# Performance work log

Measured on AMD Instinct MI355X. Metric: run time of the kernel, lower is better.

Reference implementation:

```python
import jax, jax.numpy as jnp
import numpy as np

N, M, D = 256, 64, 1024


def _l2norm(x, axis=-1, eps=1e-12):
    # tf.math.l2_normalize semantics: x / sqrt(max(sum(x^2), eps))
    sq = jnp.sum(x * x, axis=axis, keepdims=True)
    return x * jax.lax.rsqrt(jnp.maximum(sq, eps))


def setup_inputs() -> dict:
    key = jax.random.key(0)
    k1, = jax.random.split(key, 1)
    inputs = jax.random.normal(k1, (N * M, D), dtype=jnp.float32)
    w = jnp.full((1,), 10.0, dtype=jnp.float32)
    b = jnp.full((1,), -5.0, dtype=jnp.float32)
    return {"inputs": inputs, "w": w, "b": b}


def reference(inputs, w, b):
    emb = inputs.reshape(N, M, D)                       # (N, M, D)
    # speaker centroids (normalized mean over utterances)
    center = _l2norm(jnp.mean(emb, axis=1))             # (N, D)
    # leave-one-out centroid per utterance: sum over M minus self (NOT divided)
    center_except = _l2norm(jnp.sum(emb, axis=1, keepdims=True) - emb)  # (N, M, D)
    # off-diagonal similarities: every utterance vs every speaker centroid
    sim_all = jnp.einsum('jmd,id->jmi', emb, center)    # (N_utt_spk j, M, N_centroid i)
    # diagonal (i == j): utterance vs its own leave-one-out centroid
    diag = jnp.sum(center_except * emb, axis=-1)        # (N, M)
    eye = jnp.eye(N, dtype=bool)[:, None, :]            # (N, 1, N)
    sim = jnp.where(eye, diag[:, :, None], sim_all)     # (N, M, N)
    sim = w * sim + b
    return sim.reshape(N * M, N)
```

## Files before the change

### kernel.cpp

```cpp
#include <hip/hip_runtime.h>

#define NSPK 256
#define MUTT 64
#define DDIM 1024
#define NROW (NSPK * MUTT)

using frag_ab = __attribute__((ext_vector_type(8))) short;
using frag_cd = __attribute__((ext_vector_type(4))) float;

static __device__ __forceinline__ unsigned short f32_to_bf16(float f) {
    unsigned int u = __float_as_uint(f);
    return (unsigned short)((u + 0x7FFFu + ((u >> 16) & 1u)) >> 16);
}
static __device__ __forceinline__ unsigned int pack2(float a, float b) {
    return (unsigned)f32_to_bf16(a) | ((unsigned)f32_to_bf16(b) << 16);
}
static __device__ __forceinline__ void gload16(const void* g, void* l) {
    __builtin_amdgcn_global_load_lds(
        (const __attribute__((address_space(1))) unsigned int*)g,
        (__attribute__((address_space(3))) unsigned int*)l, 16, 0, 0);
}


__global__ void __launch_bounds__(256) k_prep(const float* __restrict__ emb,
                                              float* __restrict__ Sp,
                                              unsigned short* __restrict__ ebf,
                                              float* __restrict__ qg) {
    const int j = blockIdx.x;
    const int h = blockIdx.y;
    const int t = threadIdx.x;
    const int lane = t & 63, wave = t >> 6;
    const size_t rowbase = (size_t)j * MUTT + (size_t)h * 16;
    const float* src = emb + rowbase * DDIM + (size_t)t * 4;
    unsigned short* edst = ebf + rowbase * DDIM + (size_t)t * 4;
    __shared__ float qws[16][4];
    float4 s = make_float4(0.f, 0.f, 0.f, 0.f);
    #pragma unroll
    for (int m = 0; m < 16; ++m) {
        float4 v = *(const float4*)(src + (size_t)m * DDIM);
        s.x += v.x; s.y += v.y; s.z += v.z; s.w += v.w;
        float qp = v.x * v.x + v.y * v.y + v.z * v.z + v.w * v.w;
        #pragma unroll
        for (int off = 32; off > 0; off >>= 1) qp += __shfl_down(qp, off, 64);
        if (lane == 0) qws[m][wave] = qp;
        *(uint2*)(edst + (size_t)m * DDIM) = make_uint2(pack2(v.x, v.y), pack2(v.z, v.w));
    }
    __syncthreads();
    if (t < 16) qg[rowbase + t] = qws[t][0] + qws[t][1] + qws[t][2] + qws[t][3];
    *(float4*)(Sp + ((size_t)h * NSPK + j) * DDIM + (size_t)t * 4) = s;
}

template <int P>
__global__ void k_center(const float* __restrict__ Sp, unsigned short* __restrict__ cbf,
                         float* __restrict__ normS2g, float* __restrict__ normSg) {
    const int j = blockIdx.x;
    const int t = threadIdx.x;
    float4 v = make_float4(0.f, 0.f, 0.f, 0.f);
    #pragma unroll
    for (int p = 0; p < P; ++p) {
        float4 a = *(const float4*)(Sp + ((size_t)p * NSPK + j) * DDIM + (size_t)t * 4);
        v.x += a.x; v.y += a.y; v.z += a.z; v.w += a.w;
    }
    float sq = v.x * v.x + v.y * v.y + v.z * v.z + v.w * v.w;
    #pragma unroll
    for (int off = 32; off > 0; off >>= 1) sq += __shfl_down(sq, off, 64);
    __shared__ float ws[4];
    __shared__ float sc_sh;
    const int lane = t & 63, wave = t >> 6;
    if (lane == 0) ws[wave] = sq;
    __syncthreads();
    if (t == 0) {
        float tot = ws[0] + ws[1] + ws[2] + ws[3];
        normS2g[j] = tot;
        normSg[j]  = sqrtf(tot);
        float msq = tot * (1.0f / 4096.0f);
        sc_sh = rsqrtf(fmaxf(msq, 1e-12f)) * (1.0f / 64.0f);
    }
    __syncthreads();
    const float sc = sc_sh;
    *(uint2*)(cbf + (size_t)j * DDIM + (size_t)t * 4) =
        make_uint2(pack2(v.x * sc, v.y * sc), pack2(v.z * sc, v.w * sc));
}

#define RT 64
#define CT 128
#define BK 64
__global__ void __launch_bounds__(256, 2)
k_gemm2(const unsigned short* __restrict__ ebf, const unsigned short* __restrict__ cbf,
        const float* __restrict__ qg, const float* __restrict__ n2g,
        const float* __restrict__ n1g,
        const float* __restrict__ wp, const float* __restrict__ bp,
        float* __restrict__ out) {
    __shared__ unsigned short lds[2][(RT * BK + CT * BK)];

    const int tid = threadIdx.x, lane = tid & 63, wave = tid >> 6;
    const int rt = blockIdx.x;
    const int ct = blockIdx.y;
    const int row0 = rt * RT;
    const int c0 = ct * CT;
    const int jspk = rt;

    int aoff[2], boff[4];
    #pragma unroll
    for (int i = 0; i < 2; ++i) {
        int ca = i * 256 + tid;
        int row = ca >> 3, sw = ca & 7;
        aoff[i] = row * (DDIM * 2) + ((sw ^ (row & 7)) << 4);
    }
    #pragma unroll
    for (int i = 0; i < 4; ++i) {
        int cb = i * 256 + tid;
        int row = cb >> 3, sw = cb & 7;
        boff[i] = row * (DDIM * 2) + ((sw ^ (row & 7)) << 4);
    }
    const int albase = wave * 512;
    const char* agbase = (const char*)(ebf + (size_t)row0 * DDIM);
    const char* bgbase = (const char*)(cbf + (size_t)c0 * DDIM);

    const int quad = lane >> 4;
    const int m16 = lane & 15;
    const int wrow = wave >> 1, wcol = wave & 1;
    int arow[2], brow[4];
    arow[0] = wrow * 32 + m16; arow[1] = arow[0] + 16;
    #pragma unroll
    for (int cc = 0; cc < 4; ++cc) brow[cc] = wcol * 64 + cc * 16 + m16;

    frag_cd acc[2][4];
    #pragma unroll
    for (int rr = 0; rr < 2; ++rr)
        #pragma unroll
        for (int cc = 0; cc < 4; ++cc) acc[rr][cc] = (frag_cd){0.f, 0.f, 0.f, 0.f};

    #pragma unroll
    for (int i = 0; i < 2; ++i) gload16(agbase + aoff[i], &lds[0][i * 2048 + albase]);
    #pragma unroll
    for (int i = 0; i < 4; ++i) gload16(bgbase + boff[i], &lds[0][4096 + i * 2048 + albase]);
    __syncthreads();

    const int NIT = DDIM / BK;
    for (int it = 0; it < NIT; ++it) {
        const int cur = it & 1;
        if (it + 1 < NIT) {
            const char* ag = agbase + (size_t)(it + 1) * BK * 2;
            const char* bg = bgbase + (size_t)(it + 1) * BK * 2;
            unsigned short* Ln = &lds[cur ^ 1][0];
            #pragma unroll
            for (int i = 0; i < 2; ++i) gload16(ag + aoff[i], Ln + i * 2048 + albase);
            #pragma unroll
            for (int i = 0; i < 4; ++i) gload16(bg + boff[i], Ln + 4096 + i * 2048 + albase);
        }
        const unsigned short* L = &lds[cur][0];
        frag_ab af[2][2], bf[4][2];
        #pragma unroll
        for (int rr = 0; rr < 2; ++rr)
            #pragma unroll
            for (int s = 0; s < 2; ++s) {
                int addr = arow[rr] * 128 + ((((s << 2) + quad) ^ (arow[rr] & 7)) << 4);
                af[rr][s] = *(const frag_ab*)&L[addr >> 1];
            }
        #pragma unroll
        for (int cc = 0; cc < 4; ++cc)
            #pragma unroll
            for (int s = 0; s < 2; ++s) {
                int addr = 8192 + brow[cc] * 128 + ((((s << 2) + quad) ^ (brow[cc] & 7)) << 4);
                bf[cc][s] = *(const frag_ab*)&L[addr >> 1];
            }
        #pragma unroll
        for (int s = 0; s < 2; ++s)
            #pragma unroll
            for (int rr = 0; rr < 2; ++rr)
                #pragma unroll
                for (int cc = 0; cc < 4; ++cc)
                    acc[rr][cc] = __builtin_amdgcn_mfma_f32_16x16x32_bf16(
                        af[rr][s], bf[cc][s], acc[rr][cc], 0, 0, 0);
        __syncthreads();
    }

    const float wv = wp[0], bv = bp[0];
    const float ns2 = n2g[jspk], ns = n1g[jspk];
    #pragma unroll
    for (int rr = 0; rr < 2; ++rr) {
        int rbase = wrow * 32 + rr * 16 + (quad << 2);
        #pragma unroll
        for (int cc = 0; cc < 4; ++cc) {
            int col = c0 + wcol * 64 + cc * 16 + m16;
            frag_cd v = acc[rr][cc];
            #pragma unroll
            for (int r2 = 0; r2 < 4; ++r2) {
                int grow = row0 + rbase + r2;
                float val = v[r2];
                if (col == jspk) {
                    float q = qg[grow];
                    float rd = val * ns;
                    float den2 = ns2 - 2.f * rd + q;
                    val = (rd - q) * rsqrtf(fmaxf(den2, 1e-12f));
                }
                out[(size_t)grow * NSPK + col] = wv * val + bv;
            }
        }
    }
}


__global__ void k_sums(const float* __restrict__ emb, float* __restrict__ Sp) {
    const int j = blockIdx.x;
    const int h = blockIdx.y;
    const int c = threadIdx.x;
    const float* base = emb + ((size_t)j * MUTT + (size_t)h * 32) * DDIM + (size_t)c * 4;
    float4 acc = make_float4(0.f, 0.f, 0.f, 0.f);
    #pragma unroll 8
    for (int m = 0; m < 32; ++m) {
        float4 v = *(const float4*)(base + (size_t)m * DDIM);
        acc.x += v.x; acc.y += v.y; acc.z += v.z; acc.w += v.w;
    }
    *(float4*)(Sp + ((size_t)h * NSPK + j) * DDIM + (size_t)c * 4) = acc;
}

__global__ void __launch_bounds__(256)
k_gemm_old(const float* __restrict__ emb, const unsigned short* __restrict__ cbf,
           const float* __restrict__ normS2g, const float* __restrict__ normSg,
           const float* __restrict__ wp, const float* __restrict__ bp,
           float* __restrict__ out) {
    __shared__ unsigned short Asm[32][32];
    __shared__ unsigned short Bsm[256][32];
    __shared__ float qpart[32][8];
    __shared__ float qfin[32];
    const int tid = threadIdx.x, lane = tid & 63, wave = tid >> 6;
    const int row0 = blockIdx.x * 32;
    const int jspk = row0 >> 6;
    frag_cd acc[2][4];
    #pragma unroll
    for (int rr = 0; rr < 2; ++rr)
        #pragma unroll
        for (int cc = 0; cc < 4; ++cc) acc[rr][cc] = (frag_cd){0.f, 0.f, 0.f, 0.f};
    const int ar = tid >> 3, ak = (tid & 7) << 2;
    const float* aptr = emb + (size_t)(row0 + ar) * DDIM + ak;
    float qacc = 0.f;
    const int bi = tid >> 2, bk = (tid & 3) << 3;
    const int am = lane & 15, kq = (lane >> 4) << 3;
    for (int k0 = 0; k0 < DDIM; k0 += 32) {
        __syncthreads();
        float4 av = *(const float4*)(aptr + k0);
        qacc += av.x * av.x + av.y * av.y + av.z * av.z + av.w * av.w;
        *(uint2*)&Asm[ar][ak] = make_uint2(pack2(av.x, av.y), pack2(av.z, av.w));
        #pragma unroll
        for (int p = 0; p < 4; ++p) {
            int brow = p * 64 + bi;
            *(uint4*)&Bsm[brow][bk] = *(const uint4*)(cbf + (size_t)brow * DDIM + k0 + bk);
        }
        __syncthreads();
        frag_ab afr[2], bfr[4];
        #pragma unroll
        for (int rr = 0; rr < 2; ++rr) afr[rr] = *(const frag_ab*)&Asm[rr * 16 + am][kq];
        #pragma unroll
        for (int cc = 0; cc < 4; ++cc) bfr[cc] = *(const frag_ab*)&Bsm[wave * 64 + cc * 16 + am][kq];
        #pragma unroll
        for (int rr = 0; rr < 2; ++rr)
            #pragma unroll
            for (int cc = 0; cc < 4; ++cc)
                acc[rr][cc] = __builtin_amdgcn_mfma_f32_16x16x32_bf16(afr[rr], bfr[cc], acc[rr][cc], 0, 0, 0);
    }
    qpart[ar][tid & 7] = qacc;
    __syncthreads();
    if (tid < 32) {
        float s = 0.f;
        #pragma unroll
        for (int u = 0; u < 8; ++u) s += qpart[tid][u];
        qfin[tid] = s;
    }
    __syncthreads();
    const float wv = wp[0], bv = bp[0];
    const float ns2 = normS2g[jspk], ns = normSg[jspk];
    #pragma unroll
    for (int rr = 0; rr < 2; ++rr) {
        int rbase = rr * 16 + ((lane >> 4) << 2);
        #pragma unroll
        for (int cc = 0; cc < 4; ++cc) {
            int col = wave * 64 + cc * 16 + (lane & 15);
            frag_cd v = acc[rr][cc];
            #pragma unroll
            for (int r2 = 0; r2 < 4; ++r2) {
                int lrow = rbase + r2;
                float val = v[r2];
                if (col == jspk) {
                    float q = qfin[lrow];
                    float rd = val * ns;
                    float den2 = ns2 - 2.f * rd + q;
                    val = (rd - q) * rsqrtf(fmaxf(den2, 1e-12f));
                }
                out[(size_t)(row0 + lrow) * NSPK + col] = wv * val + bv;
            }
        }
    }
}

extern "C" void kernel_launch(void* const* d_in, const int* in_sizes, int n_in,
                              void* d_out, int out_size, void* d_ws, size_t ws_size,
                              hipStream_t stream) {
    const float* emb = (const float*)d_in[0];
    const float* w   = (const float*)d_in[1];
    const float* b   = (const float*)d_in[2];
    float* out = (float*)d_out;

    const size_t sz_Sp  = (size_t)4 * NSPK * DDIM * 4;
    const size_t sz_ebf = (size_t)NROW * DDIM * 2;
    const size_t sz_cbf = (size_t)NSPK * DDIM * 2;
    const size_t sz_qg  = (size_t)NROW * 4;
    const size_t need = sz_Sp + sz_ebf + sz_cbf + sz_qg + 2 * NSPK * 4;

    if (ws_size >= need) {
        char* p = (char*)d_ws;
        float* Sp = (float*)p;              p += sz_Sp;
        unsigned short* ebf = (unsigned short*)p; p += sz_ebf;
        unsigned short* cbf = (unsigned short*)p; p += sz_cbf;
        float* qg = (float*)p;              p += sz_qg;
        float* n2 = (float*)p;              p += NSPK * 4;
        float* n1 = (float*)p;
        k_prep<<<dim3(NSPK, 4), 256, 0, stream>>>(emb, Sp, ebf, qg);
        k_center<4><<<NSPK, 256, 0, stream>>>(Sp, cbf, n2, n1);
        k_gemm2<<<dim3(NROW / RT, NSPK / CT), 256, 0, stream>>>(ebf, cbf, qg, n2, n1, w, b, out);
    } else {
        float* Sp = (float*)d_ws;
        unsigned short* cbf = (unsigned short*)(Sp + 2 * NSPK * DDIM);
        float* n2 = (float*)(cbf + NSPK * DDIM);
        float* n1 = n2 + NSPK;
        k_sums<<<dim3(NSPK, 2), 256, 0, stream>>>(emb, Sp);
        k_center<2><<<NSPK, 256, 0, stream>>>(Sp, cbf, n2, n1);
        k_gemm_old<<<NROW / 32, 256, 0, stream>>>(emb, cbf, n2, n1, w, b, out);
    }
}
```

Measured before the change: 127.2 us.

## Use register-staged single LDS buffer in GEMM and restructure prep row mapping

The GEMM switches from double-buffered direct global-to-LDS loads to a single LDS buffer. The next tile is prefetched into registers during the MFMA work and written to LDS after a barrier. Halving LDS and raising launch bounds to 4 blocks per CU is meant to increase occupancy, at the cost of an extra barrier and more register pressure per iteration. The prep kernel now has each wave read whole rows with wave-local norm reductions and combines partial sums through LDS, which reduces cross-wave shuffles and syncs.

New measurement: 171.6 us. +34.9%, slower.

```diff
diff --git a/kernel.cpp b/kernel.cpp
--- a/kernel.cpp
+++ b/kernel.cpp
@@ -14,11 +14,6 @@
 }
 static __device__ __forceinline__ unsigned int pack2(float a, float b) {
     return (unsigned)f32_to_bf16(a) | ((unsigned)f32_to_bf16(b) << 16);
-}
-static __device__ __forceinline__ void gload16(const void* g, void* l) {
-    __builtin_amdgcn_global_load_lds(
-        (const __attribute__((address_space(1))) unsigned int*)g,
-        (__attribute__((address_space(3))) unsigned int*)l, 16, 0, 0);
 }
 
 
@@ -31,23 +26,46 @@
     const int t = threadIdx.x;
     const int lane = t & 63, wave = t >> 6;
     const size_t rowbase = (size_t)j * MUTT + (size_t)h * 16;
-    const float* src = emb + rowbase * DDIM + (size_t)t * 4;
-    unsigned short* edst = ebf + rowbase * DDIM + (size_t)t * 4;
-    __shared__ float qws[16][4];
-    float4 s = make_float4(0.f, 0.f, 0.f, 0.f);
-    #pragma unroll
-    for (int m = 0; m < 16; ++m) {
-        float4 v = *(const float4*)(src + (size_t)m * DDIM);
-        s.x += v.x; s.y += v.y; s.z += v.z; s.w += v.w;
-        float qp = v.x * v.x + v.y * v.y + v.z * v.z + v.w * v.w;
-        #pragma unroll
-        for (int off = 32; off > 0; off >>= 1) qp += __shfl_down(qp, off, 64);
-        if (lane == 0) qws[m][wave] = qp;
-        *(uint2*)(edst + (size_t)m * DDIM) = make_uint2(pack2(v.x, v.y), pack2(v.z, v.w));
-    }
-    __syncthreads();
-    if (t < 16) qg[rowbase + t] = qws[t][0] + qws[t][1] + qws[t][2] + qws[t][3];
-    *(float4*)(Sp + ((size_t)h * NSPK + j) * DDIM + (size_t)t * 4) = s;
+    __shared__ float sacc[4][DDIM];
+    __shared__ float qsh[16];
+
+    float4 s[4];
+    #pragma unroll
+    for (int c = 0; c < 4; ++c) s[c] = make_float4(0.f, 0.f, 0.f, 0.f);
+
+    #pragma unroll
+    for (int r = 0; r < 4; ++r) {
+        const int row = wave * 4 + r;
+        const float* src = emb + (rowbase + row) * DDIM;
+        unsigned short* dst = ebf + (rowbase + row) * DDIM;
+        float4 v[4];
+        #pragma unroll
+        for (int c = 0; c < 4; ++c)
+            v[c] = *(const float4*)(src + c * 256 + lane * 4);
+        float q = 0.f;
+        #pragma unroll
+        for (int c = 0; c < 4; ++c) {
+            s[c].x += v[c].x; s[c].y += v[c].y; s[c].z += v[c].z; s[c].w += v[c].w;
+            q += v[c].x * v[c].x + v[c].y * v[c].y + v[c].z * v[c].z + v[c].w * v[c].w;
+            *(uint2*)(dst + c * 256 + lane * 4) =
+                make_uint2(pack2(v[c].x, v[c].y), pack2(v[c].z, v[c].w));
+        }
+        #pragma unroll
+        for (int off = 32; off > 0; off >>= 1) q += __shfl_down(q, off, 64);
+        if (lane == 0) qsh[row] = q;
+    }
+    #pragma unroll
+    for (int c = 0; c < 4; ++c)
+        *(float4*)&sacc[wave][c * 256 + lane * 4] = s[c];
+    __syncthreads();
+    if (t < 16) qg[rowbase + t] = qsh[t];
+    float4 a0 = *(float4*)&sacc[0][t * 4];
+    float4 a1 = *(float4*)&sacc[1][t * 4];
+    float4 a2 = *(float4*)&sacc[2][t * 4];
+    float4 a3 = *(float4*)&sacc[3][t * 4];
+    float4 r = make_float4(a0.x + a1.x + a2.x + a3.x, a0.y + a1.y + a2.y + a3.y,
+                           a0.z + a1.z + a2.z + a3.z, a0.w + a1.w + a2.w + a3.w);
+    *(float4*)(Sp + ((size_t)h * NSPK + j) * DDIM + (size_t)t * 4) = r;
 }
 
 template <int P>
@@ -85,13 +103,13 @@
 #define RT 64
 #define CT 128
 #define BK 64
-__global__ void __launch_bounds__(256, 2)
-k_gemm2(const unsigned short* __restrict__ ebf, const unsigned short* __restrict__ cbf,
+__global__ void __launch_bounds__(256, 4)
+k_gemm3(const unsigned short* __restrict__ ebf, const unsigned short* __restrict__ cbf,
         const float* __restrict__ qg, const float* __restrict__ n2g,
         const float* __restrict__ n1g,
         const float* __restrict__ wp, const float* __restrict__ bp,
         float* __restrict__ out) {
-    __shared__ unsigned short lds[2][(RT * BK + CT * BK)];
+    __shared__ unsigned short lds[RT * BK + CT * BK];
 
     const int tid = threadIdx.x, lane = tid & 63, wave = tid >> 6;
     const int rt = blockIdx.x;
@@ -103,17 +121,14 @@
     int aoff[2], boff[4];
     #pragma unroll
     for (int i = 0; i < 2; ++i) {
-        int ca = i * 256 + tid;
-        int row = ca >> 3, sw = ca & 7;
+        int ca = i * 256 + tid, row = ca >> 3, sw = ca & 7;
         aoff[i] = row * (DDIM * 2) + ((sw ^ (row & 7)) << 4);
     }
     #pragma unroll
     for (int i = 0; i < 4; ++i) {
-        int cb = i * 256 + tid;
-        int row = cb >> 3, sw = cb & 7;
+        int cb = i * 256 + tid, row = cb >> 3, sw = cb & 7;
         boff[i] = row * (DDIM * 2) + ((sw ^ (row & 7)) << 4);
     }
-    const int albase = wave * 512;
     const char* agbase = (const char*)(ebf + (size_t)row0 * DDIM);
     const char* bgbase = (const char*)(cbf + (size_t)c0 * DDIM);
 
@@ -131,49 +146,56 @@
         #pragma unroll
         for (int cc = 0; cc < 4; ++cc) acc[rr][cc] = (frag_cd){0.f, 0.f, 0.f, 0.f};
 
-    #pragma unroll
-    for (int i = 0; i < 2; ++i) gload16(agbase + aoff[i], &lds[0][i * 2048 + albase]);
-    #pragma unroll
-    for (int i = 0; i < 4; ++i) gload16(bgbase + boff[i], &lds[0][4096 + i * 2048 + albase]);
+    uint4 pa[2], pb[4];
+    #pragma unroll
+    for (int i = 0; i < 2; ++i) pa[i] = *(const uint4*)(agbase + aoff[i]);
+    #pragma unroll
+    for (int i = 0; i < 4; ++i) pb[i] = *(const uint4*)(bgbase + boff[i]);
+    #pragma unroll
+    for (int i = 0; i < 2; ++i) *(uint4*)&lds[(i * 256 + tid) * 8] = pa[i];
+    #pragma unroll
+    for (int i = 0; i < 4; ++i) *(uint4*)&lds[RT * BK + (i * 256 + tid) * 8] = pb[i];
     __syncthreads();
 
     const int NIT = DDIM / BK;
     for (int it = 0; it < NIT; ++it) {
-        const int cur = it & 1;
         if (it + 1 < NIT) {
             const char* ag = agbase + (size_t)(it + 1) * BK * 2;
             const char* bg = bgbase + (size_t)(it + 1) * BK * 2;
-            unsigned short* Ln = &lds[cur ^ 1][0];
-            #pragma unroll
-            for (int i = 0; i < 2; ++i) gload16(ag + aoff[i], Ln + i * 2048 + albase);
-            #pragma unroll
-            for (int i = 0; i < 4; ++i) gload16(bg + boff[i], Ln + 4096 + i * 2048 + albase);
-        }
-        const unsigned short* L = &lds[cur][0];
-        frag_ab af[2][2], bf[4][2];
-        #pragma unroll
-        for (int rr = 0; rr < 2; ++rr)
-            #pragma unroll
-            for (int s = 0; s < 2; ++s) {
-                int addr = arow[rr] * 128 + ((((s << 2) + quad) ^ (arow[rr] & 7)) << 4);
-                af[rr][s] = *(const frag_ab*)&L[addr >> 1];
+            #pragma unroll
+            for (int i = 0; i < 2; ++i) pa[i] = *(const uint4*)(ag + aoff[i]);
+            #pragma unroll
+            for (int i = 0; i < 4; ++i) pb[i] = *(const uint4*)(bg + boff[i]);
+        }
+        #pragma unroll
+        for (int s = 0; s < 2; ++s) {
+            frag_ab af[2], bf[4];
+            const int kc = (s << 2) + quad;
+            #pragma unroll
+            for (int rr = 0; rr < 2; ++rr) {
+                int addr = arow[rr] * 128 + ((kc ^ (arow[rr] & 7)) << 4);
+                af[rr] = *(const frag_ab*)&lds[addr >> 1];
             }
-        #pragma unroll
-        for (int cc = 0; cc < 4; ++cc)
-            #pragma unroll
-            for (int s = 0; s < 2; ++s) {
-                int addr = 8192 + brow[cc] * 128 + ((((s << 2) + quad) ^ (brow[cc] & 7)) << 4);
-                bf[cc][s] = *(const frag_ab*)&L[addr >> 1];
+            #pragma unroll
+            for (int cc = 0; cc < 4; ++cc) {
+                int addr = (RT * BK * 2) + brow[cc] * 128 + ((kc ^ (brow[cc] & 7)) << 4);
+                bf[cc] = *(const frag_ab*)&lds[addr >> 1];
             }
-        #pragma unroll
-        for (int s = 0; s < 2; ++s)
             #pragma unroll
             for (int rr = 0; rr < 2; ++rr)
                 #pragma unroll
                 for (int cc = 0; cc < 4; ++cc)
                     acc[rr][cc] = __builtin_amdgcn_mfma_f32_16x16x32_bf16(
-                        af[rr][s], bf[cc][s], acc[rr][cc], 0, 0, 0);
+                        af[rr], bf[cc], acc[rr][cc], 0, 0, 0);
+        }
         __syncthreads();
+        if (it + 1 < NIT) {
+            #pragma unroll
+            for (int i = 0; i < 2; ++i) *(uint4*)&lds[(i * 256 + tid) * 8] = pa[i];
+            #pragma unroll
+            for (int i = 0; i < 4; ++i) *(uint4*)&lds[RT * BK + (i * 256 + tid) * 8] = pb[i];
+            __syncthreads();
+        }
     }
 
     const float wv = wp[0], bv = bp[0];
@@ -315,10 +337,10 @@
         unsigned short* cbf = (unsigned short*)p; p += sz_cbf;
         float* qg = (float*)p;              p += sz_qg;
         float* n2 = (float*)p;              p += NSPK * 4;
-        float* n1 = (float*)p;
+        float* n1 = n2 + NSPK;
         k_prep<<<dim3(NSPK, 4), 256, 0, stream>>>(emb, Sp, ebf, qg);
         k_center<4><<<NSPK, 256, 0, stream>>>(Sp, cbf, n2, n1);
-        k_gemm2<<<dim3(NROW / RT, NSPK / CT), 256, 0, stream>>>(ebf, cbf, qg, n2, n1, w, b, out);
+        k_gemm3<<<dim3(NROW / RT, NSPK / CT), 256, 0, stream>>>(ebf, cbf, qg, n2, n1, w, b, out);
     } else {
         float* Sp = (float*)d_ws;
         unsigned short* cbf = (unsigned short*)(Sp + 2 * NSPK * DDIM);
```

## Rework GEMM to stage centroids in LDS and stream embeddings from registers

Applied to the files above, without the earlier changes.

The GEMM now stages a 64-column slab of bf16 centroids into LDS, in two halves of the K dimension, and reads the embedding A fragments straight from global memory into registers. This drops the double-buffered A/B LDS pipeline and most per-iteration barriers. Each block now covers 128 rows by 64 columns, and the diagonal correction looks up the speaker per row. The prep kernel is split across 8 row-chunks per speaker to raise parallelism, which makes the partial-sum buffer larger and means the centroid kernel sums 8 partials. The risk is that unstaged global A loads add latency with no software prefetch.

Result: slower. 130.6 us (+2.7%).

```diff
diff --git a/kernel.cpp b/kernel.cpp
--- a/kernel.cpp
+++ b/kernel.cpp
@@ -30,13 +30,13 @@
     const int h = blockIdx.y;
     const int t = threadIdx.x;
     const int lane = t & 63, wave = t >> 6;
-    const size_t rowbase = (size_t)j * MUTT + (size_t)h * 16;
+    const size_t rowbase = (size_t)j * MUTT + (size_t)h * 8;
     const float* src = emb + rowbase * DDIM + (size_t)t * 4;
     unsigned short* edst = ebf + rowbase * DDIM + (size_t)t * 4;
-    __shared__ float qws[16][4];
+    __shared__ float qws[8][4];
     float4 s = make_float4(0.f, 0.f, 0.f, 0.f);
     #pragma unroll
-    for (int m = 0; m < 16; ++m) {
+    for (int m = 0; m < 8; ++m) {
         float4 v = *(const float4*)(src + (size_t)m * DDIM);
         s.x += v.x; s.y += v.y; s.z += v.z; s.w += v.w;
         float qp = v.x * v.x + v.y * v.y + v.z * v.z + v.w * v.w;
@@ -46,7 +46,7 @@
         *(uint2*)(edst + (size_t)m * DDIM) = make_uint2(pack2(v.x, v.y), pack2(v.z, v.w));
     }
     __syncthreads();
-    if (t < 16) qg[rowbase + t] = qws[t][0] + qws[t][1] + qws[t][2] + qws[t][3];
+    if (t < 8) qg[rowbase + t] = qws[t][0] + qws[t][1] + qws[t][2] + qws[t][3];
     *(float4*)(Sp + ((size_t)h * NSPK + j) * DDIM + (size_t)t * 4) = s;
 }
 
@@ -82,48 +82,24 @@
         make_uint2(pack2(v.x * sc, v.y * sc), pack2(v.z * sc, v.w * sc));
 }
 
-#define RT 64
-#define CT 128
-#define BK 64
 __global__ void __launch_bounds__(256, 2)
-k_gemm2(const unsigned short* __restrict__ ebf, const unsigned short* __restrict__ cbf,
+k_gemm5(const unsigned short* __restrict__ ebf, const unsigned short* __restrict__ cbf,
         const float* __restrict__ qg, const float* __restrict__ n2g,
         const float* __restrict__ n1g,
         const float* __restrict__ wp, const float* __restrict__ bp,
         float* __restrict__ out) {
-    __shared__ unsigned short lds[2][(RT * BK + CT * BK)];
+    __shared__ unsigned short Bs[64 * 512];
 
     const int tid = threadIdx.x, lane = tid & 63, wave = tid >> 6;
-    const int rt = blockIdx.x;
+    const int bx = blockIdx.x;
     const int ct = blockIdx.y;
-    const int row0 = rt * RT;
-    const int c0 = ct * CT;
-    const int jspk = rt;
-
-    int aoff[2], boff[4];
-    #pragma unroll
-    for (int i = 0; i < 2; ++i) {
-        int ca = i * 256 + tid;
-        int row = ca >> 3, sw = ca & 7;
-        aoff[i] = row * (DDIM * 2) + ((sw ^ (row & 7)) << 4);
-    }
-    #pragma unroll
-    for (int i = 0; i < 4; ++i) {
-        int cb = i * 256 + tid;
-        int row = cb >> 3, sw = cb & 7;
-        boff[i] = row * (DDIM * 2) + ((sw ^ (row & 7)) << 4);
-    }
-    const int albase = wave * 512;
-    const char* agbase = (const char*)(ebf + (size_t)row0 * DDIM);
-    const char* bgbase = (const char*)(cbf + (size_t)c0 * DDIM);
+    const int row0 = bx * 128;
+    const int c0 = ct * 64;
 
     const int quad = lane >> 4;
     const int m16 = lane & 15;
-    const int wrow = wave >> 1, wcol = wave & 1;
-    int arow[2], brow[4];
-    arow[0] = wrow * 32 + m16; arow[1] = arow[0] + 16;
-    #pragma unroll
-    for (int cc = 0; cc < 4; ++cc) brow[cc] = wcol * 64 + cc * 16 + m16;
+
+    const char* agbase = (const char*)ebf + ((size_t)(row0 + wave * 32 + m16) * DDIM + quad * 8) * 2;
 
     frag_cd acc[2][4];
     #pragma unroll
@@ -132,65 +108,56 @@
         for (int cc = 0; cc < 4; ++cc) acc[rr][cc] = (frag_cd){0.f, 0.f, 0.f, 0.f};
 
     #pragma unroll
-    for (int i = 0; i < 2; ++i) gload16(agbase + aoff[i], &lds[0][i * 2048 + albase]);
-    #pragma unroll
-    for (int i = 0; i < 4; ++i) gload16(bgbase + boff[i], &lds[0][4096 + i * 2048 + albase]);
-    __syncthreads();
-
-    const int NIT = DDIM / BK;
-    for (int it = 0; it < NIT; ++it) {
-        const int cur = it & 1;
-        if (it + 1 < NIT) {
-            const char* ag = agbase + (size_t)(it + 1) * BK * 2;
-            const char* bg = bgbase + (size_t)(it + 1) * BK * 2;
-            unsigned short* Ln = &lds[cur ^ 1][0];
-            #pragma unroll
-            for (int i = 0; i < 2; ++i) gload16(ag + aoff[i], Ln + i * 2048 + albase);
-            #pragma unroll
-            for (int i = 0; i < 4; ++i) gload16(bg + boff[i], Ln + 4096 + i * 2048 + albase);
-        }
-        const unsigned short* L = &lds[cur][0];
-        frag_ab af[2][2], bf[4][2];
-        #pragma unroll
-        for (int rr = 0; rr < 2; ++rr)
-            #pragma unroll
-            for (int s = 0; s < 2; ++s) {
-                int addr = arow[rr] * 128 + ((((s << 2) + quad) ^ (arow[rr] & 7)) << 4);
-                af[rr][s] = *(const frag_ab*)&L[addr >> 1];
+    for (int h = 0; h < 2; ++h) {
+        if (h) __syncthreads();
+        #pragma unroll
+        for (int round = 0; round < 16; ++round) {
+            const int col = round * 4 + wave;
+            const int s = col & 7;
+            const char* g = (const char*)cbf +
+                (size_t)(c0 + col) * (DDIM * 2) + h * 1024 + ((lane ^ s) << 4);
+            gload16(g, (char*)Bs + col * 1024 + (lane << 4));
+        }
+        __syncthreads();
+
+        #pragma unroll 4
+        for (int ks = 0; ks < 16; ++ks) {
+            frag_ab af[2], bf[4];
+            const int koff = h * 1024 + ks * 64;
+            af[0] = *(const frag_ab*)(agbase + koff);
+            af[1] = *(const frag_ab*)(agbase + 16 * (DDIM * 2) + koff);
+            #pragma unroll
+            for (int cc = 0; cc < 4; ++cc) {
+                const int col = cc * 16 + m16;
+                const int chunk = ((ks * 4 + quad) ^ (col & 7));
+                bf[cc] = *(const frag_ab*)((const char*)Bs + col * 1024 + (chunk << 4));
             }
-        #pragma unroll
-        for (int cc = 0; cc < 4; ++cc)
-            #pragma unroll
-            for (int s = 0; s < 2; ++s) {
-                int addr = 8192 + brow[cc] * 128 + ((((s << 2) + quad) ^ (brow[cc] & 7)) << 4);
-                bf[cc][s] = *(const frag_ab*)&L[addr >> 1];
-            }
-        #pragma unroll
-        for (int s = 0; s < 2; ++s)
             #pragma unroll
             for (int rr = 0; rr < 2; ++rr)
                 #pragma unroll
                 for (int cc = 0; cc < 4; ++cc)
                     acc[rr][cc] = __builtin_amdgcn_mfma_f32_16x16x32_bf16(
-                        af[rr][s], bf[cc][s], acc[rr][cc], 0, 0, 0);
-        __syncthreads();
+                        af[rr], bf[cc], acc[rr][cc], 0, 0, 0);
+        }
     }
 
     const float wv = wp[0], bv = bp[0];
-    const float ns2 = n2g[jspk], ns = n1g[jspk];
     #pragma unroll
     for (int rr = 0; rr < 2; ++rr) {
-        int rbase = wrow * 32 + rr * 16 + (quad << 2);
+        int rbase = wave * 32 + rr * 16 + (quad << 2);
         #pragma unroll
         for (int cc = 0; cc < 4; ++cc) {
-            int col = c0 + wcol * 64 + cc * 16 + m16;
+            int col = c0 + cc * 16 + m16;
             frag_cd v = acc[rr][cc];
             #pragma unroll
             for (int r2 = 0; r2 < 4; ++r2) {
                 int grow = row0 + rbase + r2;
                 float val = v[r2];
+                int jspk = grow >> 6;
                 if (col == jspk) {
                     float q = qg[grow];
+                    float ns2 = n2g[jspk];
+                    float ns = n1g[jspk];
                     float rd = val * ns;
                     float den2 = ns2 - 2.f * rd + q;
                     val = (rd - q) * rsqrtf(fmaxf(den2, 1e-12f));
@@ -302,7 +269,7 @@
     const float* b   = (const float*)d_in[2];
     float* out = (float*)d_out;
 
-    const size_t sz_Sp  = (size_t)4 * NSPK * DDIM * 4;
+    const size_t sz_Sp  = (size_t)8 * NSPK * DDIM * 4;
     const size_t sz_ebf = (size_t)NROW * DDIM * 2;
     const size_t sz_cbf = (size_t)NSPK * DDIM * 2;
     const size_t sz_qg  = (size_t)NROW * 4;
@@ -315,10 +282,10 @@
         unsigned short* cbf = (unsigned short*)p; p += sz_cbf;
         float* qg = (float*)p;              p += sz_qg;
         float* n2 = (float*)p;              p += NSPK * 4;
-        float* n1 = (float*)p;
-        k_prep<<<dim3(NSPK, 4), 256, 0, stream>>>(emb, Sp, ebf, qg);
-        k_center<4><<<NSPK, 256, 0, stream>>>(Sp, cbf, n2, n1);
-        k_gemm2<<<dim3(NROW / RT, NSPK / CT), 256, 0, stream>>>(ebf, cbf, qg, n2, n1, w, b, out);
+        float* n1 = n2 + NSPK;
+        k_prep<<<dim3(NSPK, 8), 256, 0, stream>>>(emb, Sp, ebf, qg);
+        k_center<8><<<NSPK, 256, 0, stream>>>(Sp, cbf, n2, n1);
+        k_gemm5<<<dim3(NROW / 128, NSPK / 64), 256, 0, stream>>>(ebf, cbf, qg, n2, n1, w, b, out);
     } else {
         float* Sp = (float*)d_ws;
         unsigned short* cbf = (unsigned short*)(Sp + 2 * NSPK * DDIM);
```
